# Optimization experiments

Hardware: AMD Instinct MI355X
Metric: run time of the kernel (lower is better)

The kernel has to match this reference:

```python
import jax, jax.numpy as jnp
import numpy as np

N_NODES = 10000
N_EDGES = 160000
D_IN = 50
ALPHA = 0.2  # LeakyReLU negative slope


def _xavier(key, shape):
    fan_in, fan_out = shape[0], int(np.prod(shape[1:]))
    limit = float(np.sqrt(6.0 / (fan_in + fan_out)))
    return jax.random.uniform(key, shape, jnp.float32, -limit, limit)


def setup_inputs() -> dict:
    key = jax.random.key(0)
    ks = jax.random.split(key, 8)
    x = jax.random.normal(ks[0], (N_NODES, D_IN), jnp.float32)
    edge_idx = jax.random.randint(ks[1], (2, N_EDGES), 0, N_NODES, jnp.int64)
    # layer 1: 50 -> 4 heads x 256, concat
    W1 = _xavier(ks[2], (D_IN, 4, 256))
    a1 = _xavier(ks[3], (4, 512))  # [H, 2F]: split into a_src, a_dst
    # layer 2: 1024 -> 4 heads x 256, concat
    W2 = _xavier(ks[4], (1024, 4, 256))
    a2 = _xavier(ks[5], (4, 512))
    # layer 3: 1024 -> 6 heads x 121, mean
    W3 = _xavier(ks[6], (1024, 6, 121))
    a3 = _xavier(ks[7], (6, 242))
    return {"x": x, "edge_idx": edge_idx, "W1": W1, "a1": a1,
            "W2": W2, "a2": a2, "W3": W3, "a3": a3}


def gat_layer(h, W, a, src, dst, aggregate):
    """Multi-head GAT layer over an edge list. h:[N,Din], W:[Din,H,F], a:[H,2F]."""
    N = h.shape[0]
    Wh = jnp.einsum('nd,dhf->nhf', h, W)                    # [N, H, F]
    F = Wh.shape[-1]
    att_src = jnp.einsum('nhf,hf->nh', Wh, a[:, :F])         # a^T [Wh_i || .]
    att_dst = jnp.einsum('nhf,hf->nh', Wh, a[:, F:])         # a^T [. || Wh_j]
    logits = jax.nn.leaky_relu(att_src[src] + att_dst[dst], ALPHA)  # [E, H]
    # numerically stable softmax over incoming edges of each destination node
    m = jax.ops.segment_max(logits, dst, num_segments=N)
    e = jnp.exp(logits - m[dst])
    denom = jax.ops.segment_sum(e, dst, num_segments=N)
    coef = e / (denom[dst] + 1e-16)                           # [E, H]
    out = jax.ops.segment_sum(coef[:, :, None] * Wh[src], dst, num_segments=N)
    if aggregate == 'concat':
        return out.reshape(N, -1)
    return out.mean(axis=1)


def reference(x, edge_idx, W1, a1, W2, a2, W3, a3):
    src, dst = edge_idx[0], edge_idx[1]
    h1 = jax.nn.elu(gat_layer(x, W1, a1, src, dst, 'concat'))   # [N, 1024]
    h2 = jax.nn.elu(gat_layer(h1, W2, a2, src, dst, 'concat'))  # [N, 1024]
    h3_in = h1 + h2                                              # residual skip
    return gat_layer(h3_in, W3, a3, src, dst, 'mean')            # [N, 121]
```

## Files before the change

### kernel.cpp

```cpp
#include <hip/hip_runtime.h>
#include <hip/hip_bf16.h>
#include <math.h>

#define NN 10000
#define NE 160000

typedef __attribute__((ext_vector_type(8))) _Float16 f16x8;
typedef __attribute__((ext_vector_type(4))) _Float16 f16x4;
typedef __attribute__((ext_vector_type(4))) float f32x4;

__global__ void count_kernel(const int* __restrict__ dst, int* __restrict__ counts, int E) {
  int e = blockIdx.x * blockDim.x + threadIdx.x;
  if (e < E) atomicAdd(&counts[dst[e]], 1);
}

__global__ __launch_bounds__(1024) void scan_kernel(const int* __restrict__ counts,
                                                    int* __restrict__ row_ptr,
                                                    int* __restrict__ cursor, int N) {
  __shared__ int sums[1024];
  int t = threadIdx.x;
  const int CH = (N + 1023) >> 10;
  int base = t * CH;
  int s = 0;
  for (int i = 0; i < CH; ++i) { int idx = base + i; if (idx < N) s += counts[idx]; }
  sums[t] = s;
  __syncthreads();
  for (int off = 1; off < 1024; off <<= 1) {
    int v = 0;
    if (t >= off) v = sums[t - off];
    __syncthreads();
    if (t >= off) sums[t] += v;
    __syncthreads();
  }
  int run = (t == 0) ? 0 : sums[t - 1];
  for (int i = 0; i < CH; ++i) {
    int idx = base + i;
    if (idx < N) { row_ptr[idx] = run; cursor[idx] = run; run += counts[idx]; }
  }
  if (t == 0) row_ptr[N] = sums[1023];
}

__global__ void scatter_kernel(const int* __restrict__ src, const int* __restrict__ dst,
                               int* __restrict__ cursor, int* __restrict__ ssrc, int E) {
  int e = blockIdx.x * blockDim.x + threadIdx.x;
  if (e < E) {
    int pos = atomicAdd(&cursor[dst[e]], 1);
    ssrc[pos] = src[e];
  }
}

#define SEG0 (NN * 64)
#define SEG1 (1024 * 64)
#define SEG2 (1024 * 1024)
#define SEG3 (768 * 1024)
__global__ void prep_kernel(const float* __restrict__ x, const float* __restrict__ W1,
                            const float* __restrict__ W2, const float* __restrict__ W3,
                            _Float16* __restrict__ xh, _Float16* __restrict__ w1,
                            _Float16* __restrict__ w2, _Float16* __restrict__ w3) {
  int i = blockIdx.x * blockDim.x + threadIdx.x;
  if (i < SEG0) {
    int m = i >> 6, k = i & 63;
    xh[i] = (_Float16)(k < 50 ? x[m * 50 + k] : 0.f);
  } else if (i < SEG0 + SEG1) {
    int j = i - SEG0;
    int n = j >> 6, k = j & 63;
    w1[j] = (_Float16)(k < 50 ? W1[k * 1024 + n] : 0.f);
  } else if (i < SEG0 + SEG1 + SEG2) {
    int j = i - SEG0 - SEG1;
    int n = j >> 10, k = j & 1023;
    w2[j] = (_Float16)W2[k * 1024 + n];
  } else if (i < SEG0 + SEG1 + SEG2 + SEG3) {
    int j = i - SEG0 - SEG1 - SEG2;
    int n = j >> 10, k = j & 1023;
    w3[j] = (_Float16)(n < 726 ? W3[k * 726 + n] : 0.f);
  }
}

template<int PAD121>
__global__ __launch_bounds__(256) void gemm_f16(const _Float16* __restrict__ A,
                                                const _Float16* __restrict__ B,
                                                _Float16* __restrict__ C,
                                                int M, int KP, int NcStore, int NC) {
  int flat = blockIdx.x;
  int xcd = flat & 7;
  int slot = flat >> 3;
  int cblk = slot % NC;
  int rblk = (slot / NC) * 8 + xcd;
  const int m0 = rblk * 128;
  if (m0 >= M) return;
  const int n0 = cblk * 128;

  __shared__ _Float16 As[128 * 72];
  __shared__ _Float16 Bs[128 * 72];

  const int t = threadIdx.x;
  const int lane = t & 63;
  const int wid = t >> 6;
  const int wr = wid >> 1;
  const int wc = wid & 1;
  const int row_in = lane & 15;
  const int kgrp = lane >> 4;

  f32x4 acc[4][4];
#pragma unroll
  for (int i = 0; i < 4; ++i)
#pragma unroll
    for (int j = 0; j < 4; ++j) acc[i][j] = (f32x4){0.f, 0.f, 0.f, 0.f};

  for (int k0 = 0; k0 < KP; k0 += 64) {
    if (k0) __syncthreads();
#pragma unroll
    for (int i = 0; i < 4; ++i) {
      int lin = (i * 256 + t) * 8;
      int row = lin >> 6;
      int k = lin & 63;
      int gm = m0 + row;
      if (gm >= M) gm = M - 1;
      *(f16x8*)&As[row * 72 + k] = *(const f16x8*)&A[(size_t)gm * KP + k0 + k];
      *(f16x8*)&Bs[row * 72 + k] = *(const f16x8*)&B[(size_t)(n0 + row) * KP + k0 + k];
    }
    __syncthreads();

#pragma unroll
    for (int ks = 0; ks < 64; ks += 32) {
      f16x8 a[4], b[4];
#pragma unroll
      for (int mi = 0; mi < 4; ++mi)
        a[mi] = *(const f16x8*)&As[(wr * 64 + mi * 16 + row_in) * 72 + ks + kgrp * 8];
#pragma unroll
      for (int ni = 0; ni < 4; ++ni)
        b[ni] = *(const f16x8*)&Bs[(wc * 64 + ni * 16 + row_in) * 72 + ks + kgrp * 8];
#pragma unroll
      for (int mi = 0; mi < 4; ++mi)
#pragma unroll
        for (int ni = 0; ni < 4; ++ni)
          acc[mi][ni] = __builtin_amdgcn_mfma_f32_16x16x32_f16(a[mi], b[ni], acc[mi][ni], 0, 0, 0);
    }
  }

#pragma unroll
  for (int mi = 0; mi < 4; ++mi) {
#pragma unroll
    for (int ni = 0; ni < 4; ++ni) {
      int gn = n0 + wc * 64 + ni * 16 + row_in;
      if (gn >= NcStore) continue;
#pragma unroll
      for (int j = 0; j < 4; ++j) {
        int gm = m0 + wr * 64 + mi * 16 + kgrp * 4 + j;
        if (gm >= M) continue;
        if (PAD121) {
          int h = gn / 121;
          int pc = h * 128 + (gn - h * 121);
          C[(size_t)gm * 768 + pc] = (_Float16)acc[mi][ni][j];
        } else {
          C[(size_t)gm * NcStore + gn] = (_Float16)acc[mi][ni][j];
        }
      }
    }
  }
}

template<int H, int F, int SW, int HS>
__global__ void att_kernel(const _Float16* __restrict__ Whb, const float* __restrict__ a,
                           float* __restrict__ att_s, float* __restrict__ att_d, int N) {
  int n = blockIdx.x;
  int h = threadIdx.x >> 6;
  int lane = threadIdx.x & 63;
  const _Float16* w = Whb + (size_t)n * SW + h * HS;
  const float* as = a + (size_t)h * 2 * F;
  const float* ad = as + F;
  float ss = 0.f, sd = 0.f;
  for (int f = lane; f < F; f += 64) {
    float v = (float)w[f];
    ss += v * as[f];
    sd += v * ad[f];
  }
#pragma unroll
  for (int off = 32; off > 0; off >>= 1) {
    ss += __shfl_down(ss, off);
    sd += __shfl_down(sd, off);
  }
  if (lane == 0) {
    att_s[n * H + h] = ss;
    att_d[n * H + h] = sd;
  }
}

template<int H>
__global__ __launch_bounds__(64) void edge_softmax_csr(const int* __restrict__ row_ptr,
                                                       const int* __restrict__ ssrc,
                                                       const float* __restrict__ att_s,
                                                       const float* __restrict__ att_d,
                                                       float* __restrict__ cbuf, int N) {
  int n = blockIdx.x;
  int lane = threadIdx.x;
  int beg = row_ptr[n], end = row_ptr[n + 1];
  float ad[H];
#pragma unroll
  for (int h = 0; h < H; ++h) ad[h] = att_d[n * H + h];

  float m[H];
#pragma unroll
  for (int h = 0; h < H; ++h) m[h] = -INFINITY;
  for (int k = beg + lane; k < end; k += 64) {
    int s = ssrc[k];
#pragma unroll
    for (int h = 0; h < H; ++h) {
      float x = att_s[s * H + h] + ad[h];
      float l = x >= 0.f ? x : 0.2f * x;
      m[h] = fmaxf(m[h], l);
    }
  }
#pragma unroll
  for (int h = 0; h < H; ++h)
#pragma unroll
    for (int off = 32; off > 0; off >>= 1) m[h] = fmaxf(m[h], __shfl_xor(m[h], off));

  float sum[H];
#pragma unroll
  for (int h = 0; h < H; ++h) sum[h] = 0.f;
  for (int k = beg + lane; k < end; k += 64) {
    int s = ssrc[k];
#pragma unroll
    for (int h = 0; h < H; ++h) {
      float x = att_s[s * H + h] + ad[h];
      float l = x >= 0.f ? x : 0.2f * x;
      float ev = __expf(l - m[h]);
      cbuf[(size_t)k * H + h] = ev;
      sum[h] += ev;
    }
  }
#pragma unroll
  for (int h = 0; h < H; ++h) {
#pragma unroll
    for (int off = 32; off > 0; off >>= 1) sum[h] += __shfl_xor(sum[h], off);
    sum[h] = 1.f / (sum[h] + 1e-16f);
  }
  for (int k = beg + lane; k < end; k += 64) {
#pragma unroll
    for (int h = 0; h < H; ++h) cbuf[(size_t)k * H + h] *= sum[h];
  }
}

template<int MODE>
__global__ __launch_bounds__(256) void aggregate_cat_chunk(const int* __restrict__ row_ptr,
                                                           const int* __restrict__ ssrc,
                                                           const float* __restrict__ cbuf,
                                                           const _Float16* __restrict__ Whb,
                                                           const _Float16* __restrict__ h1,
                                                           _Float16* __restrict__ outv, int N) {
  int b = blockIdx.x;
  int chunk = b & 7;
  int group = b >> 3;
  int n = group * 16 + (threadIdx.x >> 4);
  if (n >= N) return;
  int tt = threadIdx.x & 15;
  int idx = chunk * 128 + tt * 8;
  int h = chunk >> 1;

  float acc[8] = {};
  int beg = row_ptr[n], end = row_ptr[n + 1];
  int k = beg;
  for (; k + 1 < end; k += 2) {
    int s0 = ssrc[k], s1 = ssrc[k + 1];
    float c0 = cbuf[(size_t)k * 4 + h];
    float c1 = cbuf[(size_t)(k + 1) * 4 + h];
    f16x8 w0 = *(const f16x8*)&Whb[(size_t)s0 * 1024 + idx];
    f16x8 w1 = *(const f16x8*)&Whb[(size_t)s1 * 1024 + idx];
#pragma unroll
    for (int j = 0; j < 8; ++j) {
      acc[j] += c0 * (float)w0[j];
      acc[j] += c1 * (float)w1[j];
    }
  }
  if (k < end) {
    int s0 = ssrc[k];
    float c0 = cbuf[(size_t)k * 4 + h];
    f16x8 w0 = *(const f16x8*)&Whb[(size_t)s0 * 1024 + idx];
#pragma unroll
    for (int j = 0; j < 8; ++j) acc[j] += c0 * (float)w0[j];
  }

  size_t o = (size_t)n * 1024 + idx;
  f16x8 r1;
  if (MODE == 1) r1 = *(const f16x8*)&h1[o];
  f16x8 vo;
#pragma unroll
  for (int j = 0; j < 8; ++j) {
    float v = acc[j];
    v = v > 0.f ? v : expm1f(v);
    if (MODE == 1) v += (float)r1[j];
    vo[j] = (_Float16)v;
  }
  *(f16x8*)&outv[o] = vo;
}

__global__ __launch_bounds__(256) void aggregate_mean_chunk(const int* __restrict__ row_ptr,
                                                            const int* __restrict__ ssrc,
                                                            const float* __restrict__ cbuf,
                                                            const _Float16* __restrict__ Whb,
                                                            float* __restrict__ part, int N) {
  int b = blockIdx.x;
  int h = b & 7;
  if (h >= 6) return;
  int n = (b >> 3) * 16 + (threadIdx.x >> 4);
  if (n >= N) return;
  int tt = threadIdx.x & 15;
  int base = h * 128 + tt * 8;

  float acc[8] = {};
  int beg = row_ptr[n], end = row_ptr[n + 1];
  int k = beg;
  for (; k + 1 < end; k += 2) {
    int s0 = ssrc[k], s1 = ssrc[k + 1];
    float c0 = cbuf[(size_t)k * 6 + h];
    float c1 = cbuf[(size_t)(k + 1) * 6 + h];
    f16x8 w0 = *(const f16x8*)&Whb[(size_t)s0 * 768 + base];
    f16x8 w1 = *(const f16x8*)&Whb[(size_t)s1 * 768 + base];
#pragma unroll
    for (int j = 0; j < 8; ++j) {
      acc[j] += c0 * (float)w0[j];
      acc[j] += c1 * (float)w1[j];
    }
  }
  if (k < end) {
    int s0 = ssrc[k];
    float c0 = cbuf[(size_t)k * 6 + h];
    f16x8 w0 = *(const f16x8*)&Whb[(size_t)s0 * 768 + base];
#pragma unroll
    for (int j = 0; j < 8; ++j) acc[j] += c0 * (float)w0[j];
  }

  float* p = &part[(size_t)n * 768 + base];
  *(f32x4*)&p[0] = (f32x4){acc[0], acc[1], acc[2], acc[3]};
  *(f32x4*)&p[4] = (f32x4){acc[4], acc[5], acc[6], acc[7]};
}

__global__ __launch_bounds__(128) void reduce_mean(const float* __restrict__ part,
                                                   float* __restrict__ out, int N) {
  int n = blockIdx.x;
  int f = threadIdx.x;
  if (f >= 121) return;
  const float* p = &part[(size_t)n * 768];
  float s = 0.f;
#pragma unroll
  for (int h = 0; h < 6; ++h) s += p[h * 128 + f];
  out[(size_t)n * 121 + f] = s * (1.0f / 6.0f);
}

extern "C" void kernel_launch(void* const* d_in, const int* in_sizes, int n_in,
                              void* d_out, int out_size, void* d_ws, size_t ws_size,
                              hipStream_t stream) {
  const float* x  = (const float*)d_in[0];
  const int* eidx = (const int*)d_in[1];
  const float* W1 = (const float*)d_in[2];
  const float* a1 = (const float*)d_in[3];
  const float* W2 = (const float*)d_in[4];
  const float* a2 = (const float*)d_in[5];
  const float* W3 = (const float*)d_in[6];
  const float* a3 = (const float*)d_in[7];
  float* out = (float*)d_out;

  const int N = NN, E = NE;
  const int* src = eidx;
  const int* dst = eidx + E;

  char* ws = (char*)d_ws;
  size_t off = 0;
  auto alloc = [&](size_t bytes) -> void* {
    void* p = ws + off;
    off += (bytes + 255) & ~(size_t)255;
    return p;
  };
  _Float16* Whf  = (_Float16*)alloc((size_t)N * 1024 * 2);
  _Float16* h1   = (_Float16*)alloc((size_t)N * 1024 * 2);
  _Float16* hsum = (_Float16*)alloc((size_t)N * 1024 * 2);
  _Float16* xh   = (_Float16*)alloc((size_t)N * 64 * 2);
  _Float16* w1   = (_Float16*)alloc((size_t)1024 * 64 * 2);
  _Float16* w2   = (_Float16*)alloc((size_t)1024 * 1024 * 2);
  _Float16* w3   = (_Float16*)alloc((size_t)768 * 1024 * 2);
  float* cbuf  = (float*)alloc((size_t)E * 6 * 4);
  float* part  = (float*)alloc((size_t)N * 768 * 4);
  float* atts  = (float*)alloc((size_t)N * 6 * 4);
  float* attd  = (float*)alloc((size_t)N * 6 * 4);
  int* counts  = (int*)alloc((size_t)N * 4);
  int* row_ptr = (int*)alloc((size_t)(N + 1) * 4);
  int* cursor  = (int*)alloc((size_t)N * 4);
  int* ssrc    = (int*)alloc((size_t)E * 4);

  hipMemsetAsync(counts, 0, (size_t)N * 4, stream);
  prep_kernel<<<(SEG0 + SEG1 + SEG2 + SEG3 + 255) / 256, 256, 0, stream>>>(x, W1, W2, W3, xh, w1, w2, w3);
  count_kernel<<<(E + 255) / 256, 256, 0, stream>>>(dst, counts, E);
  scan_kernel<<<1, 1024, 0, stream>>>(counts, row_ptr, cursor, N);
  scatter_kernel<<<(E + 255) / 256, 256, 0, stream>>>(src, dst, cursor, ssrc, E);

  const int RPG = 10;
  const int AGG_GRID = 8 * ((N + 15) / 16);

  gemm_f16<0><<<8 * RPG * 8, 256, 0, stream>>>(xh, w1, Whf, N, 64, 1024, 8);
  att_kernel<4, 256, 1024, 256><<<N, 256, 0, stream>>>(Whf, a1, atts, attd, N);
  edge_softmax_csr<4><<<N, 64, 0, stream>>>(row_ptr, ssrc, atts, attd, cbuf, N);
  aggregate_cat_chunk<0><<<AGG_GRID, 256, 0, stream>>>(row_ptr, ssrc, cbuf, Whf, nullptr, h1, N);

  gemm_f16<0><<<8 * RPG * 8, 256, 0, stream>>>(h1, w2, Whf, N, 1024, 1024, 8);
  att_kernel<4, 256, 1024, 256><<<N, 256, 0, stream>>>(Whf, a2, atts, attd, N);
  edge_softmax_csr<4><<<N, 64, 0, stream>>>(row_ptr, ssrc, atts, attd, cbuf, N);
  aggregate_cat_chunk<1><<<AGG_GRID, 256, 0, stream>>>(row_ptr, ssrc, cbuf, Whf, h1, hsum, N);

  gemm_f16<1><<<8 * RPG * 6, 256, 0, stream>>>(hsum, w3, Whf, N, 1024, 726, 6);
  att_kernel<6, 121, 768, 128><<<N, 384, 0, stream>>>(Whf, a3, atts, attd, N);
  edge_softmax_csr<6><<<N, 64, 0, stream>>>(row_ptr, ssrc, atts, attd, cbuf, N);
  aggregate_mean_chunk<<<AGG_GRID, 256, 0, stream>>>(row_ptr, ssrc, cbuf, Whf, part, N);
  reduce_mean<<<N, 128, 0, stream>>>(part, out, N);
}
```

Measured before the change: 299.2 us.

## Use direct global-to-LDS loads with XOR swizzle in GEMM, defer softmax normalization

The GEMM now stages A and B tiles with global_load_lds (direct global-to-LDS DMA) into unpadded 64-wide rows, using an XOR swizzle to avoid LDS bank conflicts instead of padding. The edge softmax no longer rescales every edge coefficient in a second pass; it stores a per-node reciprocal denominator that the aggregate kernels multiply in at the end. The degree-count kernel is folded into the prep kernel to save a launch. These changes remove register staging traffic in the GEMM, one read-modify-write pass over the coefficient buffer, and one launch, at the cost of more complex indexing.

```diff
diff --git a/kernel.cpp b/kernel.cpp
--- a/kernel.cpp
+++ b/kernel.cpp
@@ -9,9 +9,9 @@
 typedef __attribute__((ext_vector_type(4))) _Float16 f16x4;
 typedef __attribute__((ext_vector_type(4))) float f32x4;
 
-__global__ void count_kernel(const int* __restrict__ dst, int* __restrict__ counts, int E) {
-  int e = blockIdx.x * blockDim.x + threadIdx.x;
-  if (e < E) atomicAdd(&counts[dst[e]], 1);
+static __device__ __forceinline__ void gload_lds16(const _Float16* g, _Float16* l) {
+  __builtin_amdgcn_global_load_lds((const __attribute__((address_space(1))) char*)g,
+                                   (__attribute__((address_space(3))) char*)l, 16, 0, 0);
 }
 
 __global__ __launch_bounds__(1024) void scan_kernel(const int* __restrict__ counts,
@@ -49,38 +49,49 @@
   }
 }
 
-#define SEG0 (NN * 64)
-#define SEG1 (1024 * 64)
-#define SEG2 (1024 * 1024)
-#define SEG3 (768 * 1024)
+#define P0 (NN * 64)
+#define P1 (1024 * 64)
+#define P2 (1024 * 1024)
+#define P3 (768 * 1024)
+#define P4 NE
 __global__ void prep_kernel(const float* __restrict__ x, const float* __restrict__ W1,
                             const float* __restrict__ W2, const float* __restrict__ W3,
+                            const int* __restrict__ dst, int* __restrict__ counts,
                             _Float16* __restrict__ xh, _Float16* __restrict__ w1,
                             _Float16* __restrict__ w2, _Float16* __restrict__ w3) {
   int i = blockIdx.x * blockDim.x + threadIdx.x;
-  if (i < SEG0) {
+  if (i < P0) {
     int m = i >> 6, k = i & 63;
     xh[i] = (_Float16)(k < 50 ? x[m * 50 + k] : 0.f);
-  } else if (i < SEG0 + SEG1) {
-    int j = i - SEG0;
-    int n = j >> 6, k = j & 63;
-    w1[j] = (_Float16)(k < 50 ? W1[k * 1024 + n] : 0.f);
-  } else if (i < SEG0 + SEG1 + SEG2) {
-    int j = i - SEG0 - SEG1;
-    int n = j >> 10, k = j & 1023;
-    w2[j] = (_Float16)W2[k * 1024 + n];
-  } else if (i < SEG0 + SEG1 + SEG2 + SEG3) {
-    int j = i - SEG0 - SEG1 - SEG2;
-    int n = j >> 10, k = j & 1023;
-    w3[j] = (_Float16)(n < 726 ? W3[k * 726 + n] : 0.f);
-  }
+    return;
+  }
+  i -= P0;
+  if (i < P1) {
+    int n = i >> 6, k = i & 63;
+    w1[i] = (_Float16)(k < 50 ? W1[k * 1024 + n] : 0.f);
+    return;
+  }
+  i -= P1;
+  if (i < P2) {
+    int n = i >> 10, k = i & 1023;
+    w2[i] = (_Float16)W2[k * 1024 + n];
+    return;
+  }
+  i -= P2;
+  if (i < P3) {
+    int n = i >> 10, k = i & 1023;
+    w3[i] = (_Float16)(n < 726 ? W3[k * 726 + n] : 0.f);
+    return;
+  }
+  i -= P3;
+  if (i < P4) atomicAdd(&counts[dst[i]], 1);
 }
 
 template<int PAD121>
 __global__ __launch_bounds__(256) void gemm_f16(const _Float16* __restrict__ A,
                                                 const _Float16* __restrict__ B,
                                                 _Float16* __restrict__ C,
-                                                int M, int KP, int NcStore, int NC) {
+                                                int M, int KP, int NC) {
   int flat = blockIdx.x;
   int xcd = flat & 7;
   int slot = flat >> 3;
@@ -90,8 +101,8 @@
   if (m0 >= M) return;
   const int n0 = cblk * 128;
 
-  __shared__ _Float16 As[128 * 72];
-  __shared__ _Float16 Bs[128 * 72];
+  __shared__ _Float16 As[128 * 64];
+  __shared__ _Float16 Bs[128 * 64];
 
   const int t = threadIdx.x;
   const int lane = t & 63;
@@ -101,6 +112,9 @@
   const int row_in = lane & 15;
   const int kgrp = lane >> 4;
 
+  const int srow = wid * 32 + ((lane >> 3) & 7);
+  const int sl7 = lane & 7;
+
   f32x4 acc[4][4];
 #pragma unroll
   for (int i = 0; i < 4; ++i)
@@ -110,26 +124,33 @@
   for (int k0 = 0; k0 < KP; k0 += 64) {
     if (k0) __syncthreads();
 #pragma unroll
-    for (int i = 0; i < 4; ++i) {
-      int lin = (i * 256 + t) * 8;
-      int row = lin >> 6;
-      int k = lin & 63;
+    for (int j = 0; j < 4; ++j) {
+      int row = srow + j * 8;
+      int gs = (sl7 ^ (row & 7)) * 8;
       int gm = m0 + row;
       if (gm >= M) gm = M - 1;
-      *(f16x8*)&As[row * 72 + k] = *(const f16x8*)&A[(size_t)gm * KP + k0 + k];
-      *(f16x8*)&Bs[row * 72 + k] = *(const f16x8*)&B[(size_t)(n0 + row) * KP + k0 + k];
+      _Float16* ldsA = &As[(wid * 32 + j * 8) * 64];
+      _Float16* ldsB = &Bs[(wid * 32 + j * 8) * 64];
+      gload_lds16(&A[(size_t)gm * KP + k0 + gs], ldsA);
+      gload_lds16(&B[(size_t)(n0 + row) * KP + k0 + gs], ldsB);
     }
     __syncthreads();
 
 #pragma unroll
-    for (int ks = 0; ks < 64; ks += 32) {
+    for (int ks = 0; ks < 2; ++ks) {
       f16x8 a[4], b[4];
 #pragma unroll
-      for (int mi = 0; mi < 4; ++mi)
-        a[mi] = *(const f16x8*)&As[(wr * 64 + mi * 16 + row_in) * 72 + ks + kgrp * 8];
-#pragma unroll
-      for (int ni = 0; ni < 4; ++ni)
-        b[ni] = *(const f16x8*)&Bs[(wc * 64 + ni * 16 + row_in) * 72 + ks + kgrp * 8];
+      for (int mi = 0; mi < 4; ++mi) {
+        int arow = wr * 64 + mi * 16 + row_in;
+        int ps = ((kgrp + ks * 4) ^ (arow & 7)) * 8;
+        a[mi] = *(const f16x8*)&As[arow * 64 + ps];
+      }
+#pragma unroll
+      for (int ni = 0; ni < 4; ++ni) {
+        int brow = wc * 64 + ni * 16 + row_in;
+        int ps = ((kgrp + ks * 4) ^ (brow & 7)) * 8;
+        b[ni] = *(const f16x8*)&Bs[brow * 64 + ps];
+      }
 #pragma unroll
       for (int mi = 0; mi < 4; ++mi)
 #pragma unroll
@@ -143,17 +164,18 @@
 #pragma unroll
     for (int ni = 0; ni < 4; ++ni) {
       int gn = n0 + wc * 64 + ni * 16 + row_in;
-      if (gn >= NcStore) continue;
 #pragma unroll
       for (int j = 0; j < 4; ++j) {
         int gm = m0 + wr * 64 + mi * 16 + kgrp * 4 + j;
         if (gm >= M) continue;
         if (PAD121) {
-          int h = gn / 121;
-          int pc = h * 128 + (gn - h * 121);
-          C[(size_t)gm * 768 + pc] = (_Float16)acc[mi][ni][j];
+          if (gn < 726) {
+            int h = gn / 121;
+            int pc = h * 128 + (gn - h * 121);
+            C[(size_t)gm * 768 + pc] = (_Float16)acc[mi][ni][j];
+          }
         } else {
-          C[(size_t)gm * NcStore + gn] = (_Float16)acc[mi][ni][j];
+          C[(size_t)gm * 1024 + gn] = (_Float16)acc[mi][ni][j];
         }
       }
     }
@@ -191,7 +213,8 @@
                                                        const int* __restrict__ ssrc,
                                                        const float* __restrict__ att_s,
                                                        const float* __restrict__ att_d,
-                                                       float* __restrict__ cbuf, int N) {
+                                                       float* __restrict__ cbuf,
+                                                       float* __restrict__ dinv, int N) {
   int n = blockIdx.x;
   int lane = threadIdx.x;
   int beg = row_ptr[n], end = row_ptr[n + 1];
@@ -234,18 +257,15 @@
   for (int h = 0; h < H; ++h) {
 #pragma unroll
     for (int off = 32; off > 0; off >>= 1) sum[h] += __shfl_xor(sum[h], off);
-    sum[h] = 1.f / (sum[h] + 1e-16f);
-  }
-  for (int k = beg + lane; k < end; k += 64) {
-#pragma unroll
-    for (int h = 0; h < H; ++h) cbuf[(size_t)k * H + h] *= sum[h];
-  }
+  }
+  if (lane < H) dinv[n * H + lane] = 1.f / (sum[lane] + 1e-16f);
 }
 
 template<int MODE>
 __global__ __launch_bounds__(256) void aggregate_cat_chunk(const int* __restrict__ row_ptr,
                                                            const int* __restrict__ ssrc,
                                                            const float* __restrict__ cbuf,
+                                                           const float* __restrict__ dinv,
                                                            const _Float16* __restrict__ Whb,
                                                            const _Float16* __restrict__ h1,
                                                            _Float16* __restrict__ outv, int N) {
@@ -257,6 +277,7 @@
   int tt = threadIdx.x & 15;
   int idx = chunk * 128 + tt * 8;
   int h = chunk >> 1;
+  float inv = dinv[n * 4 + h];
 
   float acc[8] = {};
   int beg = row_ptr[n], end = row_ptr[n + 1];
@@ -287,7 +308,7 @@
   f16x8 vo;
 #pragma unroll
   for (int j = 0; j < 8; ++j) {
-    float v = acc[j];
+    float v = acc[j] * inv;
     v = v > 0.f ? v : expm1f(v);
     if (MODE == 1) v += (float)r1[j];
     vo[j] = (_Float16)v;
@@ -298,6 +319,7 @@
 __global__ __launch_bounds__(256) void aggregate_mean_chunk(const int* __restrict__ row_ptr,
                                                             const int* __restrict__ ssrc,
                                                             const float* __restrict__ cbuf,
+                                                            const float* __restrict__ dinv,
                                                             const _Float16* __restrict__ Whb,
                                                             float* __restrict__ part, int N) {
   int b = blockIdx.x;
@@ -307,6 +329,7 @@
   if (n >= N) return;
   int tt = threadIdx.x & 15;
   int base = h * 128 + tt * 8;
+  float inv = dinv[n * 6 + h];
 
   float acc[8] = {};
   int beg = row_ptr[n], end = row_ptr[n + 1];
@@ -332,8 +355,8 @@
   }
 
   float* p = &part[(size_t)n * 768 + base];
-  *(f32x4*)&p[0] = (f32x4){acc[0], acc[1], acc[2], acc[3]};
-  *(f32x4*)&p[4] = (f32x4){acc[4], acc[5], acc[6], acc[7]};
+  *(f32x4*)&p[0] = (f32x4){acc[0] * inv, acc[1] * inv, acc[2] * inv, acc[3] * inv};
+  *(f32x4*)&p[4] = (f32x4){acc[4] * inv, acc[5] * inv, acc[6] * inv, acc[7] * inv};
 }
 
 __global__ __launch_bounds__(128) void reduce_mean(const float* __restrict__ part,
@@ -383,33 +406,34 @@
   float* part  = (float*)alloc((size_t)N * 768 * 4);
   float* atts  = (float*)alloc((size_t)N * 6 * 4);
   float* attd  = (float*)alloc((size_t)N * 6 * 4);
+  float* dinv  = (float*)alloc((size_t)N * 6 * 4);
   int* counts  = (int*)alloc((size_t)N * 4);
   int* row_ptr = (int*)alloc((size_t)(N + 1) * 4);
   int* cursor  = (int*)alloc((size_t)N * 4);
   int* ssrc    = (int*)alloc((size_t)E * 4);
 
   hipMemsetAsync(counts, 0, (size_t)N * 4, stream);
-  prep_kernel<<<(SEG0 + SEG1 + SEG2 + SEG3 + 255) / 256, 256, 0, stream>>>(x, W1, W2, W3, xh, w1, w2, w3);
-  count_kernel<<<(E + 255) / 256, 256, 0, stream>>>(dst, counts, E);
+  const int PTOT = P0 + P1 + P2 + P3 + P4;
+  prep_kernel<<<(PTOT + 255) / 256, 256, 0, stream>>>(x, W1, W2, W3, dst, counts, xh, w1, w2, w3);
   scan_kernel<<<1, 1024, 0, stream>>>(counts, row_ptr, cursor, N);
   scatter_kernel<<<(E + 255) / 256, 256, 0, stream>>>(src, dst, cursor, ssrc, E);
 
   const int RPG = 10;
   const int AGG_GRID = 8 * ((N + 15) / 16);
 
-  gemm_f16<0><<<8 * RPG * 8, 256, 0, stream>>>(xh, w1, Whf, N, 64, 1024, 8);
+  gemm_f16<0><<<8 * RPG * 8, 256, 0, stream>>>(xh, w1, Whf, N, 64, 8);
   att_kernel<4, 256, 1024, 256><<<N, 256, 0, stream>>>(Whf, a1, atts, attd, N);
-  edge_softmax_csr<4><<<N, 64, 0, stream>>>(row_ptr, ssrc, atts, attd, cbuf, N);
-  aggregate_cat_chunk<0><<<AGG_GRID, 256, 0, stream>>>(row_ptr, ssrc, cbuf, Whf, nullptr, h1, N);
-
-  gemm_f16<0><<<8 * RPG * 8, 256, 0, stream>>>(h1, w2, Whf, N, 1024, 1024, 8);
+  edge_softmax_csr<4><<<N, 64, 0, stream>>>(row_ptr, ssrc, atts, attd, cbuf, dinv, N);
+  aggregate_cat_chunk<0><<<AGG_GRID, 256, 0, stream>>>(row_ptr, ssrc, cbuf, dinv, Whf, nullptr, h1, N);
+
+  gemm_f16<0><<<8 * RPG * 8, 256, 0, stream>>>(h1, w2, Whf, N, 1024, 8);
   att_kernel<4, 256, 1024, 256><<<N, 256, 0, stream>>>(Whf, a2, atts, attd, N);
-  edge_softmax_csr<4><<<N, 64, 0, stream>>>(row_ptr, ssrc, atts, attd, cbuf, N);
-  aggregate_cat_chunk<1><<<AGG_GRID, 256, 0, stream>>>(row_ptr, ssrc, cbuf, Whf, h1, hsum, N);
-
-  gemm_f16<1><<<8 * RPG * 6, 256, 0, stream>>>(hsum, w3, Whf, N, 1024, 726, 6);
+  edge_softmax_csr<4><<<N, 64, 0, stream>>>(row_ptr, ssrc, atts, attd, cbuf, dinv, N);
+  aggregate_cat_chunk<1><<<AGG_GRID, 256, 0, stream>>>(row_ptr, ssrc, cbuf, dinv, Whf, h1, hsum, N);
+
+  gemm_f16<1><<<8 * RPG * 6, 256, 0, stream>>>(hsum, w3, Whf, N, 1024, 6);
   att_kernel<6, 121, 768, 128><<<N, 384, 0, stream>>>(Whf, a3, atts, attd, N);
-  edge_softmax_csr<6><<<N, 64, 0, stream>>>(row_ptr, ssrc, atts, attd, cbuf, N);
-  aggregate_mean_chunk<<<AGG_GRID, 256, 0, stream>>>(row_ptr, ssrc, cbuf, Whf, part, N);
+  edge_softmax_csr<6><<<N, 64, 0, stream>>>(row_ptr, ssrc, atts, attd, cbuf, dinv, N);
+  aggregate_mean_chunk<<<AGG_GRID, 256, 0, stream>>>(row_ptr, ssrc, cbuf, dinv, Whf, part, N);
   reduce_mean<<<N, 128, 0, stream>>>(part, out, N);
 }
```

After: 289.3 us. -3.3%, faster.
